# Performance work log

Measured on AMD Instinct MI355X. Metric: run time of the kernel, lower is better.

Reference implementation:

```python
import jax, jax.numpy as jnp
import numpy as np

E, W, C, D, F = 8, 8, 1024, 512, 2048  # local experts, world_size, capacity, d_model, d_ff


def setup_inputs() -> dict:
    key = jax.random.key(0)
    k1, k2, k3 = jax.random.split(key, 3)
    x = jax.random.normal(k1, (E, W, C, D), dtype=jnp.float32)
    cap = jax.random.randint(jax.random.fold_in(key, 7), (E,), 0, C)
    wi = jax.random.normal(k2, (E, D, F), dtype=jnp.float32) * 0.02
    wo = jax.random.normal(k3, (E, F, D), dtype=jnp.float32) * 0.02
    return {
        "dispatched_hidden_states": x,
        "experts_capacity_usage": cap,
        "wi": wi,
        "wo": wo,
    }


def reference(dispatched_hidden_states, experts_capacity_usage, wi, wo):
    # LocalExperts (handle_by_capacity=False): each expert e applies its own
    # T5 FFN to its chunk x[e]; expressed as a grouped GEMM over the expert axis.
    h = jnp.einsum("ewcd,edf->ewcf", dispatched_hidden_states, wi)  # [E,W,C,F]
    h = jax.nn.relu(h)
    out = jnp.einsum("ewcf,efd->ewcd", h, wo)  # [E,W,C,D]
    return out
```

## Files before the change

### kernel.cpp

```cpp
#include <hip/hip_runtime.h>
#include <hip/hip_bf16.h>
#include <stdint.h>


#define E_N 8
#define W_N 8
#define C_N 1024
#define D_N 512
#define F_N 2048
#define ME  (W_N * C_N)

typedef __attribute__((ext_vector_type(4))) float f32x4;
typedef __attribute__((ext_vector_type(8))) short s16x8;

#define BAR()  __builtin_amdgcn_s_barrier()
#define SBAR() __builtin_amdgcn_sched_barrier(0)
#define LGKM0() do { asm volatile("s_waitcnt lgkmcnt(0)" ::: "memory"); SBAR(); } while (0)
#define VM8()   do { asm volatile("s_waitcnt vmcnt(8)"   ::: "memory"); SBAR(); } while (0)
#define VM0()   do { asm volatile("s_waitcnt vmcnt(0)"   ::: "memory"); SBAR(); } while (0)

__device__ __forceinline__ unsigned short f2bf(float f) {
  union { float f; unsigned int u; } v; v.f = f;
  unsigned int u = v.u + 0x7fffu + ((v.u >> 16) & 1u);
  return (unsigned short)(u >> 16);
}

__device__ __forceinline__ void gload_lds16(void* lds, const void* g) {
  __builtin_amdgcn_global_load_lds(
      (const __attribute__((address_space(1))) unsigned int*)g,
      (__attribute__((address_space(3))) unsigned int*)lds, 16, 0, 0);
}

__global__ __launch_bounds__(256)
void transpose_cvt(const float* __restrict__ in, unsigned short* __restrict__ out,
                   int R, int Ccols) {
  __shared__ unsigned short tile[64][65];
  const int e = blockIdx.z;
  const float* ip = in + (size_t)e * R * Ccols;
  unsigned short* op = out + (size_t)e * R * Ccols;
  const int c0 = blockIdx.x * 64, r0 = blockIdx.y * 64;
  const int t = threadIdx.x;
  const int cl = (t & 15) * 4, rw = t >> 4;
#pragma unroll
  for (int i = 0; i < 4; ++i) {
    int row = rw + i * 16;
    float4 v = *(const float4*)&ip[(size_t)(r0 + row) * Ccols + c0 + cl];
    tile[row][cl + 0] = f2bf(v.x);
    tile[row][cl + 1] = f2bf(v.y);
    tile[row][cl + 2] = f2bf(v.z);
    tile[row][cl + 3] = f2bf(v.w);
  }
  __syncthreads();
#pragma unroll
  for (int i = 0; i < 4; ++i) {
    int oc = rw + i * 16;
    ushort4 o;
    o.x = tile[cl + 0][oc];
    o.y = tile[cl + 1][oc];
    o.z = tile[cl + 2][oc];
    o.w = tile[cl + 3][oc];
    *(ushort4*)&op[(size_t)(c0 + oc) * R + r0 + cl] = o;
  }
}

__global__ __launch_bounds__(256)
void cvt_x_kernel(const float* __restrict__ in, unsigned short* __restrict__ out, size_t n) {
  size_t idx = ((size_t)blockIdx.x * 256 + threadIdx.x) * 8;
  const size_t stride = (size_t)gridDim.x * 256 * 8;
  for (; idx < n; idx += stride) {
    float4 a = *(const float4*)&in[idx];
    float4 b = *(const float4*)&in[idx + 4];
    union { s16x8 v; unsigned short u[8]; } p;
    p.u[0] = f2bf(a.x); p.u[1] = f2bf(a.y); p.u[2] = f2bf(a.z); p.u[3] = f2bf(a.w);
    p.u[4] = f2bf(b.x); p.u[5] = f2bf(b.y); p.u[6] = f2bf(b.z); p.u[7] = f2bf(b.w);
    *(s16x8*)&out[idx] = p.v;
  }
}

template<bool RELU_BF16_OUT>
__global__ __launch_bounds__(512, 2)
void gemm256p(const unsigned short* __restrict__ Abase,
              const unsigned short* __restrict__ Btbase,
              void* __restrict__ Cv, int N, int K, int nT,
              size_t aStrideE, size_t bStrideE, size_t cStrideE) {
  extern __shared__ unsigned short lds[];
  unsigned char* ldsb = (unsigned char*)lds;
  const int blk = blockIdx.x;
  const int e  = blk & 7;
  const int bi = blk >> 3;
  const int TS = nT;
  const int n0 = (bi % nT) * 256;
  const int ms = bi / nT;
  const int tid  = threadIdx.x;
  const int lane = tid & 63;
  const int wave = tid >> 6;
  const int wm = wave >> 2;
  const int wn = wave & 3;
  const unsigned short* A  = Abase  + (size_t)e * aStrideE;
  const unsigned short* Bt = Btbase + (size_t)e * bStrideE;

  const int NK = K >> 6;
  const int kshift = __builtin_ctz(NK);
  const int total = TS * NK;

  const int rl = lane & 15;
  const int gb = lane >> 4;
  const int g16_0 = ((0 * 4 + gb) ^ (rl & 7)) * 16;
  const int g16_1 = ((1 * 4 + gb) ^ (rl & 7)) * 16;
  const int aBase0 = wm * 16384 + rl * 128;
  const int bBase0 = 32768 + (wn >> 1) * 16384 + ((wn & 1) * 64 + rl) * 128;

  int rA0[2], rB0[2];
#pragma unroll
  for (int o = 0; o < 2; ++o) {
    int G = o * 512 + tid;
    int r = G >> 3;
    int gl = (G & 7) ^ (r & 7);
    rA0[o] = r * K + gl * 8;
    rB0[o] = (n0 + r) * K + gl * 8;
  }
  auto stageA = [&](int g, int h) {
    const int ktl = g & (NK - 1);
    const int buf = g & 1;
    const int m0t = (ms * TS + (g >> kshift)) * 256;
    const unsigned short* An = A + (size_t)m0t * K;
#pragma unroll
    for (int o = 0; o < 2; ++o)
      gload_lds16(ldsb + buf * 65536 + h * 16384 + o * 8192 + wave * 1024,
                  An + rA0[o] + h * 128 * K + ktl * 64);
  };
  auto stageB = [&](int g, int h) {
    const int ktl = g & (NK - 1);
    const int buf = g & 1;
#pragma unroll
    for (int o = 0; o < 2; ++o)
      gload_lds16(ldsb + buf * 65536 + 32768 + h * 16384 + o * 8192 + wave * 1024,
                  Bt + rB0[o] + h * 128 * K + ktl * 64);
  };

  f32x4 acc[8][4] = {};

  auto run_ktile = [&](int buf, int gN, bool more, bool needDrain) {
    const int bufOff = buf * 65536;
    s16x8 afr[4][2], b01[2][2], b23[2][2];
#pragma unroll
    for (int mi = 0; mi < 4; ++mi) {
      afr[mi][0] = *(const s16x8*)(ldsb + bufOff + aBase0 + mi * 2048 + g16_0);
      afr[mi][1] = *(const s16x8*)(ldsb + bufOff + aBase0 + mi * 2048 + g16_1);
    }
#pragma unroll
    for (int ni = 0; ni < 2; ++ni) {
      b01[ni][0] = *(const s16x8*)(ldsb + bufOff + bBase0 + ni * 2048 + g16_0);
      b01[ni][1] = *(const s16x8*)(ldsb + bufOff + bBase0 + ni * 2048 + g16_1);
    }
    BAR(); LGKM0();
    __builtin_amdgcn_s_setprio(1);
#pragma unroll
    for (int mi = 0; mi < 4; ++mi)
#pragma unroll
      for (int ni = 0; ni < 2; ++ni) {
        acc[mi][ni] = __builtin_amdgcn_mfma_f32_16x16x32_bf16(afr[mi][0], b01[ni][0], acc[mi][ni], 0, 0, 0);
        acc[mi][ni] = __builtin_amdgcn_mfma_f32_16x16x32_bf16(afr[mi][1], b01[ni][1], acc[mi][ni], 0, 0, 0);
      }
    __builtin_amdgcn_s_setprio(0);
    BAR();
#pragma unroll
    for (int ni = 0; ni < 2; ++ni) {
      b23[ni][0] = *(const s16x8*)(ldsb + bufOff + bBase0 + (2 + ni) * 2048 + g16_0);
      b23[ni][1] = *(const s16x8*)(ldsb + bufOff + bBase0 + (2 + ni) * 2048 + g16_1);
    }
    BAR(); LGKM0();
    __builtin_amdgcn_s_setprio(1);
#pragma unroll
    for (int mi = 0; mi < 4; ++mi)
#pragma unroll
      for (int ni = 0; ni < 2; ++ni) {
        acc[mi][2 + ni] = __builtin_amdgcn_mfma_f32_16x16x32_bf16(afr[mi][0], b23[ni][0], acc[mi][2 + ni], 0, 0, 0);
        acc[mi][2 + ni] = __builtin_amdgcn_mfma_f32_16x16x32_bf16(afr[mi][1], b23[ni][1], acc[mi][2 + ni], 0, 0, 0);
      }
    __builtin_amdgcn_s_setprio(0);
    BAR();
#pragma unroll
    for (int mi = 0; mi < 4; ++mi) {
      afr[mi][0] = *(const s16x8*)(ldsb + bufOff + aBase0 + (4 + mi) * 2048 + g16_0);
      afr[mi][1] = *(const s16x8*)(ldsb + bufOff + aBase0 + (4 + mi) * 2048 + g16_1);
    }
    if (more) { stageB(gN, 0); stageB(gN, 1); }
    BAR(); LGKM0();
    __builtin_amdgcn_s_setprio(1);
#pragma unroll
    for (int mi = 0; mi < 4; ++mi)
#pragma unroll
      for (int ni = 0; ni < 2; ++ni) {
        acc[4 + mi][2 + ni] = __builtin_amdgcn_mfma_f32_16x16x32_bf16(afr[mi][0], b23[ni][0], acc[4 + mi][2 + ni], 0, 0, 0);
        acc[4 + mi][2 + ni] = __builtin_amdgcn_mfma_f32_16x16x32_bf16(afr[mi][1], b23[ni][1], acc[4 + mi][2 + ni], 0, 0, 0);
      }
    __builtin_amdgcn_s_setprio(0);
    BAR();
    if (more) { stageA(gN, 0); stageA(gN, 1); }
    BAR();
    __builtin_amdgcn_s_setprio(1);
#pragma unroll
    for (int mi = 0; mi < 4; ++mi)
#pragma unroll
      for (int ni = 0; ni < 2; ++ni) {
        acc[4 + mi][ni] = __builtin_amdgcn_mfma_f32_16x16x32_bf16(afr[mi][0], b01[ni][0], acc[4 + mi][ni], 0, 0, 0);
        acc[4 + mi][ni] = __builtin_amdgcn_mfma_f32_16x16x32_bf16(afr[mi][1], b01[ni][1], acc[4 + mi][ni], 0, 0, 0);
      }
    __builtin_amdgcn_s_setprio(0);
    if (more) { VM8(); } else if (needDrain) { VM0(); }
    BAR();
  };

  stageB(0, 0); stageB(0, 1); stageA(0, 0); stageA(0, 1);
  stageB(1, 0); stageB(1, 1); stageA(1, 0); stageA(1, 1);
  VM8();
  BAR();

  const int rq = (lane >> 4) * 4;
  const int cq = lane & 15;

  for (int g = 0; g < total; g += 2) {
    run_ktile(0, g + 2, (g + 2 < total), true);
    run_ktile(1, g + 3, (g + 3 < total), false);
    if (((g + 2) & (NK - 1)) == 0) {
      const int m0 = (ms * TS + (g >> kshift)) * 256;
      if (RELU_BF16_OUT) {
        unsigned short* Cb = (unsigned short*)Cv + (size_t)e * cStrideE;
#pragma unroll
        for (int mi = 0; mi < 8; ++mi)
#pragma unroll
          for (int ni = 0; ni < 4; ++ni) {
            int row0 = m0 + wm * 128 + mi * 16 + rq;
            int col  = n0 + wn * 64 + ni * 16 + cq;
#pragma unroll
            for (int r = 0; r < 4; ++r) {
              float v = acc[mi][ni][r];
              v = v > 0.f ? v : 0.f;
              Cb[(size_t)(row0 + r) * N + col] = f2bf(v);
            }
          }
      } else {
        float* Cf = (float*)Cv + (size_t)e * cStrideE;
#pragma unroll
        for (int mi = 0; mi < 8; ++mi)
#pragma unroll
          for (int ni = 0; ni < 4; ++ni) {
            int row0 = m0 + wm * 128 + mi * 16 + rq;
            int col  = n0 + wn * 64 + ni * 16 + cq;
#pragma unroll
            for (int r = 0; r < 4; ++r)
              Cf[(size_t)(row0 + r) * N + col] = acc[mi][ni][r];
          }
      }
#pragma unroll
      for (int mi = 0; mi < 8; ++mi)
#pragma unroll
        for (int ni = 0; ni < 4; ++ni)
          acc[mi][ni] = (f32x4){0.f, 0.f, 0.f, 0.f};
    }
  }
}

__global__ __launch_bounds__(256)
void fused_naive(const float* __restrict__ x, const float* __restrict__ wi,
                 const float* __restrict__ wo, float* __restrict__ out) {
  __shared__ float xs[D_N];
  __shared__ float hs[F_N];
  const size_t row = blockIdx.x;
  const int e = (int)(row / (W_N * C_N));
  const float* xr = x + row * D_N;
  const float* wie = wi + (size_t)e * D_N * F_N;
  const float* woe = wo + (size_t)e * F_N * D_N;
  const int t = threadIdx.x;
  for (int d = t; d < D_N; d += 256) xs[d] = xr[d];
  __syncthreads();
  for (int f = t; f < F_N; f += 256) {
    float a = 0.f;
    for (int d = 0; d < D_N; ++d) a += xs[d] * wie[(size_t)d * F_N + f];
    hs[f] = a > 0.f ? a : 0.f;
  }
  __syncthreads();
  float* orow = out + row * D_N;
  for (int d = t; d < D_N; d += 256) {
    float a = 0.f;
    for (int f = 0; f < F_N; ++f) a += hs[f] * woe[(size_t)f * D_N + d];
    orow[d] = a;
  }
}

extern "C" void kernel_launch(void* const* d_in, const int* in_sizes, int n_in,
                              void* d_out, int out_size, void* d_ws, size_t ws_size,
                              hipStream_t stream) {
  const float* x  = (const float*)d_in[0];
  const float* wi = (const float*)d_in[2];
  const float* wo = (const float*)d_in[3];
  float* out = (float*)d_out;

  const size_t WT   = (size_t)E_N * D_N * F_N;
  unsigned short* wiT = (unsigned short*)d_ws;
  unsigned short* woT = wiT + WT;
  unsigned short* P   = woT + WT;
  const size_t baseB = 2 * WT * 2;
  const size_t XB_B  = (size_t)E_N * ME * D_N * 2;
  const size_t HF_B  = (size_t)E_N * ME * F_N * 2;

  const dim3 blk(256);
  if (ws_size >= baseB + XB_B + HF_B) {
    hipFuncSetAttribute(reinterpret_cast<const void*>(gemm256p<true>),
                        hipFuncAttributeMaxDynamicSharedMemorySize, 131072);
    hipFuncSetAttribute(reinterpret_cast<const void*>(gemm256p<false>),
                        hipFuncAttributeMaxDynamicSharedMemorySize, 131072);
    transpose_cvt<<<dim3(F_N / 64, D_N / 64, E_N), blk, 0, stream>>>(wi, wiT, D_N, F_N);
    transpose_cvt<<<dim3(D_N / 64, F_N / 64, E_N), blk, 0, stream>>>(wo, woT, F_N, D_N);
    unsigned short* xb = P;
    unsigned short* h  = P + XB_B / 2;
    cvt_x_kernel<<<2048, blk, 0, stream>>>(x, xb, (size_t)E_N * ME * D_N);
    gemm256p<true><<<dim3(256), dim3(512), 131072, stream>>>(
        xb, wiT, h, F_N, D_N, F_N / 256,
        (size_t)ME * D_N, (size_t)F_N * D_N, (size_t)ME * F_N);
    gemm256p<false><<<dim3(256), dim3(512), 131072, stream>>>(
        h, woT, out, D_N, F_N, D_N / 256,
        (size_t)ME * F_N, (size_t)D_N * F_N, (size_t)ME * D_N);
  } else {
    fused_naive<<<dim3(E_N * W_N * C_N), blk, 0, stream>>>(x, wi, wo, out);
  }
}
```

Baseline: 356.5 us.

## Fuse fp32-to-bf16 activation conversion into first GEMM's A-tile staging

Removes the separate cvt_x kernel and the bf16 copy of x. The first GEMM now loads fp32 A tiles into registers one stage ahead, converts them with packed bf16 conversion, and writes them to LDS. B tiles still use direct global-to-LDS loads. This removes a full read/write pass over x, but it raises register pressure and adds VALU and LDS-write work inside the pipelined main loop, and it reads twice as many A bytes from global memory.

```diff
diff --git a/kernel.cpp b/kernel.cpp
--- a/kernel.cpp
+++ b/kernel.cpp
@@ -1,6 +1,7 @@
 #include <hip/hip_runtime.h>
 #include <hip/hip_bf16.h>
 #include <stdint.h>
+#include <type_traits>
 
 
 #define E_N 8
@@ -15,8 +16,11 @@
 
 #define BAR()  __builtin_amdgcn_s_barrier()
 #define SBAR() __builtin_amdgcn_sched_barrier(0)
+#define CFENCE() do { asm volatile("" ::: "memory"); SBAR(); } while (0)
 #define LGKM0() do { asm volatile("s_waitcnt lgkmcnt(0)" ::: "memory"); SBAR(); } while (0)
+#define VM12()  do { asm volatile("s_waitcnt vmcnt(12)"  ::: "memory"); SBAR(); } while (0)
 #define VM8()   do { asm volatile("s_waitcnt vmcnt(8)"   ::: "memory"); SBAR(); } while (0)
+#define VM4()   do { asm volatile("s_waitcnt vmcnt(4)"   ::: "memory"); SBAR(); } while (0)
 #define VM0()   do { asm volatile("s_waitcnt vmcnt(0)"   ::: "memory"); SBAR(); } while (0)
 
 __device__ __forceinline__ unsigned short f2bf(float f) {
@@ -63,23 +67,9 @@
   }
 }
 
-__global__ __launch_bounds__(256)
-void cvt_x_kernel(const float* __restrict__ in, unsigned short* __restrict__ out, size_t n) {
-  size_t idx = ((size_t)blockIdx.x * 256 + threadIdx.x) * 8;
-  const size_t stride = (size_t)gridDim.x * 256 * 8;
-  for (; idx < n; idx += stride) {
-    float4 a = *(const float4*)&in[idx];
-    float4 b = *(const float4*)&in[idx + 4];
-    union { s16x8 v; unsigned short u[8]; } p;
-    p.u[0] = f2bf(a.x); p.u[1] = f2bf(a.y); p.u[2] = f2bf(a.z); p.u[3] = f2bf(a.w);
-    p.u[4] = f2bf(b.x); p.u[5] = f2bf(b.y); p.u[6] = f2bf(b.z); p.u[7] = f2bf(b.w);
-    *(s16x8*)&out[idx] = p.v;
-  }
-}
-
-template<bool RELU_BF16_OUT>
+template<bool A_F32, bool RELU_BF16_OUT>
 __global__ __launch_bounds__(512, 2)
-void gemm256p(const unsigned short* __restrict__ Abase,
+void gemm256p(const void* __restrict__ Abase,
               const unsigned short* __restrict__ Btbase,
               void* __restrict__ Cv, int N, int K, int nT,
               size_t aStrideE, size_t bStrideE, size_t cStrideE) {
@@ -96,7 +86,8 @@
   const int wave = tid >> 6;
   const int wm = wave >> 2;
   const int wn = wave & 3;
-  const unsigned short* A  = Abase  + (size_t)e * aStrideE;
+  const float*          Af = (const float*)Abase + (size_t)e * aStrideE;
+  const unsigned short* Ab = (const unsigned short*)Abase + (size_t)e * aStrideE;
   const unsigned short* Bt = Btbase + (size_t)e * bStrideE;
 
   const int NK = K >> 6;
@@ -123,7 +114,7 @@
     const int ktl = g & (NK - 1);
     const int buf = g & 1;
     const int m0t = (ms * TS + (g >> kshift)) * 256;
-    const unsigned short* An = A + (size_t)m0t * K;
+    const unsigned short* An = Ab + (size_t)m0t * K;
 #pragma unroll
     for (int o = 0; o < 2; ++o)
       gload_lds16(ldsb + buf * 65536 + h * 16384 + o * 8192 + wave * 1024,
@@ -138,10 +129,43 @@
                   Bt + rB0[o] + h * 128 * K + ktl * 64);
   };
 
+  f32x4 areg0[8], areg1[8];
+  auto loadA = [&](f32x4 (&ar)[8], int g) {
+    const int ktl = g & (NK - 1);
+    const int m0t = (ms * TS + (g >> kshift)) * 256;
+    const float* An = Af + (size_t)m0t * K + ktl * 64;
+#pragma unroll
+    for (int h = 0; h < 2; ++h)
+#pragma unroll
+      for (int o = 0; o < 2; ++o) {
+        const float* src = An + (size_t)(h * 128) * K + rA0[o];
+        ar[(h * 2 + o) * 2 + 0] = *(const f32x4*)src;
+        ar[(h * 2 + o) * 2 + 1] = *(const f32x4*)(src + 4);
+      }
+  };
+  auto writeA = [&](f32x4 (&ar)[8], int bufWOff) {
+#pragma unroll
+    for (int h = 0; h < 2; ++h)
+#pragma unroll
+      for (int o = 0; o < 2; ++o) {
+        f32x4 lo4 = ar[(h * 2 + o) * 2 + 0];
+        f32x4 hi4 = ar[(h * 2 + o) * 2 + 1];
+        uint4 Wd;
+        asm("v_cvt_pk_bf16_f32 %0, %1, %2" : "=v"(Wd.x) : "v"(lo4[0]), "v"(lo4[1]));
+        asm("v_cvt_pk_bf16_f32 %0, %1, %2" : "=v"(Wd.y) : "v"(lo4[2]), "v"(lo4[3]));
+        asm("v_cvt_pk_bf16_f32 %0, %1, %2" : "=v"(Wd.z) : "v"(hi4[0]), "v"(hi4[1]));
+        asm("v_cvt_pk_bf16_f32 %0, %1, %2" : "=v"(Wd.w) : "v"(hi4[2]), "v"(hi4[3]));
+        *(uint4*)(ldsb + bufWOff + h * 16384 + o * 8192 + tid * 16) = Wd;
+      }
+  };
+
   f32x4 acc[8][4] = {};
 
-  auto run_ktile = [&](int buf, int gN, bool more, bool needDrain) {
-    const int bufOff = buf * 65536;
+  auto run_ktile = [&](auto bufc, int gStage, int gWrite) {
+    constexpr int BUF = decltype(bufc)::value;
+    const int bufOff = BUF * 65536;
+    const bool moreS = gStage < total;
+    const bool moreW = gWrite < total;
     s16x8 afr[4][2], b01[2][2], b23[2][2];
 #pragma unroll
     for (int mi = 0; mi < 4; ++mi) {
@@ -185,7 +209,7 @@
       afr[mi][0] = *(const s16x8*)(ldsb + bufOff + aBase0 + (4 + mi) * 2048 + g16_0);
       afr[mi][1] = *(const s16x8*)(ldsb + bufOff + aBase0 + (4 + mi) * 2048 + g16_1);
     }
-    if (more) { stageB(gN, 0); stageB(gN, 1); }
+    if (moreS) { stageB(gStage, 0); stageB(gStage, 1); }
     BAR(); LGKM0();
     __builtin_amdgcn_s_setprio(1);
 #pragma unroll
@@ -197,7 +221,14 @@
       }
     __builtin_amdgcn_s_setprio(0);
     BAR();
-    if (more) { stageA(gN, 0); stageA(gN, 1); }
+    if (A_F32) {
+      if (moreS) {
+        if (BUF == 0) loadA(areg0, gStage); else loadA(areg1, gStage);
+      }
+      CFENCE();
+    } else {
+      if (moreS) { stageA(gStage, 0); stageA(gStage, 1); }
+    }
     BAR();
     __builtin_amdgcn_s_setprio(1);
 #pragma unroll
@@ -208,21 +239,41 @@
         acc[4 + mi][ni] = __builtin_amdgcn_mfma_f32_16x16x32_bf16(afr[mi][1], b01[ni][1], acc[4 + mi][ni], 0, 0, 0);
       }
     __builtin_amdgcn_s_setprio(0);
-    if (more) { VM8(); } else if (needDrain) { VM0(); }
-    BAR();
-  };
-
-  stageB(0, 0); stageB(0, 1); stageA(0, 0); stageA(0, 1);
-  stageB(1, 0); stageB(1, 1); stageA(1, 0); stageA(1, 1);
-  VM8();
-  BAR();
+    if (A_F32) {
+      if (moreW) {
+        if (moreS) { VM12(); } else { VM0(); }
+        if (BUF == 0) writeA(areg1, 0 * 65536 + (1) * 65536);
+        else          writeA(areg0, 0);
+        LGKM0();
+      }
+    } else {
+      if (moreS) { VM8(); } else if (moreW) { VM0(); }
+    }
+    BAR();
+  };
+
+  if (A_F32) {
+    stageB(0, 0); stageB(0, 1); CFENCE();
+    loadA(areg0, 0);            CFENCE();
+    stageB(1, 0); stageB(1, 1); CFENCE();
+    VM4();
+    writeA(areg0, 0);
+    loadA(areg1, 1); CFENCE();
+    LGKM0();
+    BAR();
+  } else {
+    stageB(0, 0); stageB(0, 1); stageA(0, 0); stageA(0, 1);
+    stageB(1, 0); stageB(1, 1); stageA(1, 0); stageA(1, 1);
+    VM8();
+    BAR();
+  }
 
   const int rq = (lane >> 4) * 4;
   const int cq = lane & 15;
 
   for (int g = 0; g < total; g += 2) {
-    run_ktile(0, g + 2, (g + 2 < total), true);
-    run_ktile(1, g + 3, (g + 3 < total), false);
+    run_ktile(std::integral_constant<int, 0>{}, g + 2, g + 1);
+    run_ktile(std::integral_constant<int, 1>{}, g + 3, g + 2);
     if (((g + 2) & (NK - 1)) == 0) {
       const int m0 = (ms * TS + (g >> kshift)) * 256;
       if (RELU_BF16_OUT) {
@@ -231,13 +282,13 @@
         for (int mi = 0; mi < 8; ++mi)
 #pragma unroll
           for (int ni = 0; ni < 4; ++ni) {
-            int row0 = m0 + wm * 128 + mi * 16 + rq;
-            int col  = n0 + wn * 64 + ni * 16 + cq;
+            int rbase = m0 + wm * 128 + mi * 16 + rq;
+            int col   = n0 + wn * 64 + ni * 16 + cq;
 #pragma unroll
             for (int r = 0; r < 4; ++r) {
               float v = acc[mi][ni][r];
               v = v > 0.f ? v : 0.f;
-              Cb[(size_t)(row0 + r) * N + col] = f2bf(v);
+              Cb[(size_t)(rbase + r) * N + col] = f2bf(v);
             }
           }
       } else {
@@ -246,11 +297,11 @@
         for (int mi = 0; mi < 8; ++mi)
 #pragma unroll
           for (int ni = 0; ni < 4; ++ni) {
-            int row0 = m0 + wm * 128 + mi * 16 + rq;
-            int col  = n0 + wn * 64 + ni * 16 + cq;
+            int rbase = m0 + wm * 128 + mi * 16 + rq;
+            int col   = n0 + wn * 64 + ni * 16 + cq;
 #pragma unroll
             for (int r = 0; r < 4; ++r)
-              Cf[(size_t)(row0 + r) * N + col] = acc[mi][ni][r];
+              Cf[(size_t)(rbase + r) * N + col] = acc[mi][ni][r];
           }
       }
 #pragma unroll
@@ -302,24 +353,21 @@
   unsigned short* woT = wiT + WT;
   unsigned short* P   = woT + WT;
   const size_t baseB = 2 * WT * 2;
-  const size_t XB_B  = (size_t)E_N * ME * D_N * 2;
   const size_t HF_B  = (size_t)E_N * ME * F_N * 2;
 
   const dim3 blk(256);
-  if (ws_size >= baseB + XB_B + HF_B) {
-    hipFuncSetAttribute(reinterpret_cast<const void*>(gemm256p<true>),
+  if (ws_size >= baseB + HF_B) {
+    hipFuncSetAttribute(reinterpret_cast<const void*>(gemm256p<true, true>),
                         hipFuncAttributeMaxDynamicSharedMemorySize, 131072);
-    hipFuncSetAttribute(reinterpret_cast<const void*>(gemm256p<false>),
+    hipFuncSetAttribute(reinterpret_cast<const void*>(gemm256p<false, false>),
                         hipFuncAttributeMaxDynamicSharedMemorySize, 131072);
     transpose_cvt<<<dim3(F_N / 64, D_N / 64, E_N), blk, 0, stream>>>(wi, wiT, D_N, F_N);
     transpose_cvt<<<dim3(D_N / 64, F_N / 64, E_N), blk, 0, stream>>>(wo, woT, F_N, D_N);
-    unsigned short* xb = P;
-    unsigned short* h  = P + XB_B / 2;
-    cvt_x_kernel<<<2048, blk, 0, stream>>>(x, xb, (size_t)E_N * ME * D_N);
-    gemm256p<true><<<dim3(256), dim3(512), 131072, stream>>>(
-        xb, wiT, h, F_N, D_N, F_N / 256,
+    unsigned short* h = P;
+    gemm256p<true, true><<<dim3(256), dim3(512), 131072, stream>>>(
+        x, wiT, h, F_N, D_N, F_N / 256,
         (size_t)ME * D_N, (size_t)F_N * D_N, (size_t)ME * F_N);
-    gemm256p<false><<<dim3(256), dim3(512), 131072, stream>>>(
+    gemm256p<false, false><<<dim3(256), dim3(512), 131072, stream>>>(
         h, woT, out, D_N, F_N, D_N / 256,
         (size_t)ME * F_N, (size_t)D_N * F_N, (size_t)ME * D_N);
   } else {
```

Result: slower. 580.6 us (+62.9%).
